# Optimization experiments

Hardware: AMD Instinct MI355X
Metric: run time of the kernel (lower is better)

The kernel has to match this reference:

```python
import jax, jax.numpy as jnp
import numpy as np

D = 1024          # embeddings_dims
HS = 128          # head_size = D // no_of_q_heads(=8)
NKV = 2           # hardcoded self.no_of_kv_heads = 2 (number of query Linear layers)


def apply_rope(x):
    # x: [..., T, d]; pairs of adjacent elements rotated (faithful to RotaryEmbeddings)
    d = x.shape[-1]
    T = x.shape[-2]
    positions = jnp.arange(0, d, 2, dtype=jnp.float32)           # step-2 positions (as in source)
    theta = 10000.0 ** (-2.0 * positions / d)                    # [d/2]
    angles = jnp.arange(T, dtype=jnp.float32)[:, None] * theta[None, :]  # [T, d/2]
    cos, sin = jnp.cos(angles), jnp.sin(angles)
    xr = x.reshape(x.shape[:-1] + (d // 2, 2))
    out = jnp.stack([xr[..., 0] * cos - xr[..., 1] * sin,
                     xr[..., 1] * cos + xr[..., 0] * sin], axis=-1)
    return out.reshape(x.shape)


def setup_inputs() -> dict:
    key = jax.random.key(0)
    k1, k2, k3, k4, k5 = jax.random.split(key, 5)
    B, T = 4, 2048
    x = jax.random.normal(k1, (B, T, D), dtype=jnp.float32)
    s = 1.0 / np.sqrt(D)
    Wq = jax.random.normal(k2, (NKV, HS, D), dtype=jnp.float32) * s  # 2 query Linear layers [out,in]
    Wk = jax.random.normal(k3, (HS, D), dtype=jnp.float32) * s
    Wv = jax.random.normal(k4, (HS, D), dtype=jnp.float32) * s
    Wo = jax.random.normal(k5, (D, NKV * HS), dtype=jnp.float32) * (1.0 / np.sqrt(NKV * HS))
    return {"x": x, "Wq": Wq, "Wk": Wk, "Wv": Wv, "Wo": Wo}


def reference(x, Wq, Wk, Wv, Wo):
    B, T, _ = x.shape
    k = apply_rope(x @ Wk.T)                              # [B,T,HS]
    v = x @ Wv.T                                          # [B,T,HS]
    q = jnp.einsum('btd,hkd->bhtk', x, Wq)                # [B,2,T,HS]
    q = apply_rope(q)
    scale = HS ** (-0.5)
    scores = jnp.einsum('bhtk,bsk->bhts', q, k) * scale   # [B,2,T,T]
    causal = jnp.tril(jnp.ones((T, T), dtype=bool))
    scores = jnp.where(causal, scores, -jnp.inf)
    w = jax.nn.softmax(scores, axis=-1)                   # dropout is identity at eval
    out = jnp.einsum('bhts,bsk->bhtk', w, v)              # [B,2,T,HS]
    out = out.transpose(0, 2, 1, 3).reshape(B, T, NKV * HS)  # concat heads on last dim
    return out @ Wo.T                                     # [B,T,D]
```

## Files before the change

kernel.cpp:

```cpp
#include <hip/hip_runtime.h>
#include <math.h>

#define DD 1024
#define HSZ 128
#define NB 4
#define TT 2048

typedef __attribute__((ext_vector_type(8))) short bf16x8;
typedef __attribute__((ext_vector_type(4))) float f32x4;

typedef __attribute__((address_space(3))) unsigned int lds_u32_t;
typedef __attribute__((address_space(1))) unsigned int glb_u32_t;

__device__ inline void gll16(const void* g, void* l) {
    __builtin_amdgcn_global_load_lds((const glb_u32_t*)g, (lds_u32_t*)l, 16, 0, 0);
}

__device__ inline unsigned short f2bf(float f){
    unsigned u = __builtin_bit_cast(unsigned, f);
    u += 0x7fff + ((u >> 16) & 1);
    return (unsigned short)(u >> 16);
}

__global__ __launch_bounds__(256) void prep_kernel(
    const float* __restrict__ Wq, const float* __restrict__ Wk,
    const float* __restrict__ Wv, const float* __restrict__ Wo,
    unsigned short* __restrict__ Wbp, unsigned short* __restrict__ Wop,
    float2* __restrict__ tab)
{
    int bid = blockIdx.x, tid = threadIdx.x;
    if (bid < 512) {
        int i = bid * 256 + tid;
        int t = i >> 6, j = i & 63;
        float theta = __powf(10000.f, -(float)j * (1.f / 32.f));
        float ang = (float)t * theta;
        tab[i] = make_float2(__cosf(ang), __sinf(ang));
        return;
    }
    const float* s;
    unsigned short* dst;
    if (bid < 768) {
        int gc = (bid - 512) * 256 + tid;
        int tileid = gc >> 10;
        int ct = tileid >> 4, kk = tileid & 15;
        int ch = gc & 1023;
        int ns = ch >> 7, kc = (ch >> 6) & 1, l6 = ch & 63;
        int wrow = ct * 128 + ns * 16 + (l6 & 15);
        int kcol = kk * 64 + kc * 32 + (l6 >> 4) * 8;
        s = (wrow < 256) ? Wq + (size_t)wrow * DD
          : (wrow < 384) ? Wk + (size_t)(wrow - 256) * DD
                         : Wv + (size_t)(wrow - 384) * DD;
        s += kcol;
        dst = Wbp + (size_t)gc * 8;
    } else {
        int gc = (bid - 768) * 256 + tid;
        int tileid = gc >> 10;
        int ct = tileid >> 2, kk = tileid & 3;
        int ch = gc & 1023;
        int ns = ch >> 7, kc = (ch >> 6) & 1, l6 = ch & 63;
        int orow = ct * 128 + ns * 16 + (l6 & 15);
        int kcol = kk * 64 + kc * 32 + (l6 >> 4) * 8;
        s = Wo + (size_t)orow * 256 + kcol;
        dst = Wop + (size_t)gc * 8;
    }
    float4 a = ((const float4*)s)[0];
    float4 c = ((const float4*)s)[1];
    unsigned short o[8] = {f2bf(a.x),f2bf(a.y),f2bf(a.z),f2bf(a.w),
                           f2bf(c.x),f2bf(c.y),f2bf(c.z),f2bf(c.w)};
    *(uint4*)dst = *(const uint4*)o;
}

__global__ __launch_bounds__(256) void qkv_gemm_kernel(
    const float* __restrict__ x,
    const unsigned short* __restrict__ Wbp,
    const float2* __restrict__ tab,
    unsigned short* __restrict__ qo,
    unsigned short* __restrict__ Kp,
    unsigned short* __restrict__ Vp)
{
    int bid = blockIdx.x;
    int rt = bid & 127, ct = bid >> 7;
    int row0 = rt * 64;
    int b = row0 >> 11, t0 = row0 & (TT - 1);
    int tid = threadIdx.x;
    int wave = tid >> 6, lane = tid & 63;
    int mrow = lane & 15, quad = lane >> 4;

    __shared__ unsigned short Bs[2][8192];

    f32x4 acc[8];
    #pragma unroll
    for (int ns = 0; ns < 8; ++ns)
        #pragma unroll
        for (int r = 0; r < 4; ++r) acc[ns][r] = 0.f;

    const float* xrow = x + (size_t)(row0 + wave * 16 + mrow) * DD;

    {
        const unsigned short* wt = Wbp + (size_t)(ct * 16) * 8192;
        #pragma unroll
        for (int u = 0; u < 4; ++u)
            gll16(wt + (size_t)(u * 256 + tid) * 8, &Bs[0][(u * 256 + (tid & 192)) * 8]);
    }

    for (int kk = 0; kk < 16; ++kk) {
        __syncthreads();
        if (kk < 15) {
            const unsigned short* wt = Wbp + (size_t)(ct * 16 + kk + 1) * 8192;
            #pragma unroll
            for (int u = 0; u < 4; ++u)
                gll16(wt + (size_t)(u * 256 + tid) * 8, &Bs[(kk + 1) & 1][(u * 256 + (tid & 192)) * 8]);
        }
        bf16x8 af[2];
        #pragma unroll
        for (int kc = 0; kc < 2; ++kc) {
            const float* s = xrow + kk * 64 + kc * 32 + quad * 8;
            float4 f0 = ((const float4*)s)[0];
            float4 f1 = ((const float4*)s)[1];
            bf16x8 pk;
            pk[0]=(short)f2bf(f0.x); pk[1]=(short)f2bf(f0.y); pk[2]=(short)f2bf(f0.z); pk[3]=(short)f2bf(f0.w);
            pk[4]=(short)f2bf(f1.x); pk[5]=(short)f2bf(f1.y); pk[6]=(short)f2bf(f1.z); pk[7]=(short)f2bf(f1.w);
            af[kc] = pk;
        }
        const unsigned short* Bcur = Bs[kk & 1];
        #pragma unroll
        for (int kc = 0; kc < 2; ++kc)
            #pragma unroll
            for (int ns = 0; ns < 8; ++ns) {
                bf16x8 bb = *(const bf16x8*)(Bcur + ((ns * 2 + kc) * 64 + lane) * 8);
                acc[ns] = __builtin_amdgcn_mfma_f32_16x16x32_bf16(af[kc], bb, acc[ns], 0, 0, 0);
            }
    }

    __syncthreads();

    if (ct < 2) {
        unsigned short* dst = qo + (size_t)(b * 2 + ct) * TT * HSZ;
        #pragma unroll
        for (int ns = 0; ns < 8; ++ns) {
            int colloc = ns * 16 + mrow;
            int pj = colloc >> 1;
            #pragma unroll
            for (int r = 0; r < 4; ++r) {
                int t = t0 + wave * 16 + quad * 4 + r;
                float v = acc[ns][r];
                float vp = __shfl_xor(v, 1, 64);
                float2 cs = tab[t * 64 + pj];
                float outv = ((mrow & 1) == 0) ? (v * cs.x - vp * cs.y)
                                               : (v * cs.x + vp * cs.y);
                dst[(size_t)t * HSZ + colloc] = f2bf(outv);
            }
        }
    } else if (ct == 2) {
        unsigned short* A_ = (unsigned short*)Bs;
        #pragma unroll
        for (int ns = 0; ns < 8; ++ns) {
            int colloc = ns * 16 + mrow;
            int pj = colloc >> 1;
            int chunk = (ns >> 1) * 4 + wave;
            int lph = (ns & 1) * 2 + (mrow >> 3);
            #pragma unroll
            for (int r = 0; r < 4; ++r) {
                int t = t0 + wave * 16 + quad * 4 + r;
                float v = acc[ns][r];
                float vp = __shfl_xor(v, 1, 64);
                float2 cs = tab[t * 64 + pj];
                float outv = ((mrow & 1) == 0) ? (v * cs.x - vp * cs.y)
                                               : (v * cs.x + vp * cs.y);
                A_[chunk * 512 + (lph * 16 + quad * 4 + r) * 8 + (mrow & 7)] = f2bf(outv);
            }
        }
        __syncthreads();
        unsigned short* kd = Kp + (size_t)(b * 32 + (t0 >> 6)) * 8192;
        #pragma unroll
        for (int u = 0; u < 4; ++u)
            *(uint4*)(kd + (u * 256 + tid) * 8) = *(const uint4*)(A_ + (u * 256 + tid) * 8);
    } else {
        unsigned short* A_ = (unsigned short*)Bs;
        #pragma unroll
        for (int ns = 0; ns < 8; ++ns) {
            int chunk = ns * 2 + (wave >> 1);
            int lanep = ((wave & 1) * 2 + (quad >> 1)) * 16 + mrow;
            #pragma unroll
            for (int r = 0; r < 4; ++r)
                A_[chunk * 512 + lanep * 8 + (quad & 1) * 4 + r] = f2bf(acc[ns][r]);
        }
        __syncthreads();
        unsigned short* vd = Vp + (size_t)(b * 32 + (t0 >> 6)) * 8192;
        #pragma unroll
        for (int u = 0; u < 4; ++u)
            *(uint4*)(vd + (u * 256 + tid) * 8) = *(const uint4*)(A_ + (u * 256 + tid) * 8);
    }
}

__global__ __launch_bounds__(256, 2) void attn_mfma_kernel(
    const unsigned short* __restrict__ q,
    const unsigned short* __restrict__ Kp,
    const unsigned short* __restrict__ Vp,
    unsigned short* __restrict__ att)
{
    int bid = blockIdx.x;
    int qt = 63 - (bid >> 3);
    int bh = bid & 7;
    int b = bh >> 1, h = bh & 1;
    int q0 = qt * 32;
    int tid = threadIdx.x;
    int wave = tid >> 6, lane = tid & 63;
    int mrow = lane & 15, quad = lane >> 4;

    __shared__ char raw[66304];
    unsigned short* Psb = (unsigned short*)raw;
    float* Os  = (float*)(raw + 16384);
    float* Ms_ = (float*)(raw + 65536);
    float* Ls_ = Ms_ + 96;

    const unsigned short* qbase = q + (((size_t)(b * 2 + h)) * TT + q0 + mrow) * HSZ + quad * 8;
    bf16x8 qf[2][4];
    #pragma unroll
    for (int u = 0; u < 2; ++u)
        #pragma unroll
        for (int c = 0; c < 4; ++c)
            qf[u][c] = *(const bf16x8*)(qbase + u * 16 * HSZ + 32 * c);

    float mrun[2][4], lrun[2][4];
    f32x4 O[2][8];
    #pragma unroll
    for (int u = 0; u < 2; ++u) {
        #pragma unroll
        for (int r = 0; r < 4; ++r) { mrun[u][r] = -1e30f; lrun[u][r] = 0.f; }
        #pragma unroll
        for (int g = 0; g < 8; ++g)
            #pragma unroll
            for (int r = 0; r < 4; ++r) O[u][g][r] = 0.f;
    }

    const int NT = (qt >> 1) + 1;
    const float scl = 0.08838834764831845f;
    unsigned short* Pw = Psb + wave * 2048;

    for (int j = wave; j < NT; j += 4) {
        const unsigned short* Kt = Kp + (size_t)(b * 32 + j) * 8192;
        const unsigned short* Vt = Vp + (size_t)(b * 32 + j) * 8192;
        int s0 = j * 64;

        f32x4 S[2][4];
        #pragma unroll
        for (int u = 0; u < 2; ++u)
            #pragma unroll
            for (int f = 0; f < 4; ++f)
                #pragma unroll
                for (int r = 0; r < 4; ++r) S[u][f][r] = 0.f;

        #pragma unroll
        for (int c = 0; c < 4; ++c)
            #pragma unroll
            for (int f = 0; f < 4; ++f) {
                bf16x8 bk = *(const bf16x8*)(Kt + ((c * 4 + f) * 64 + lane) * 8);
                S[0][f] = __builtin_amdgcn_mfma_f32_16x16x32_bf16(qf[0][c], bk, S[0][f], 0, 0, 0);
                S[1][f] = __builtin_amdgcn_mfma_f32_16x16x32_bf16(qf[1][c], bk, S[1][f], 0, 0, 0);
            }

        if (j == NT - 1) {
            #pragma unroll
            for (int u = 0; u < 2; ++u)
                #pragma unroll
                for (int f = 0; f < 4; ++f) {
                    int sg = s0 + 16 * f + mrow;
                    #pragma unroll
                    for (int r = 0; r < 4; ++r) {
                        int qg = q0 + u * 16 + quad * 4 + r;
                        S[u][f][r] = (sg <= qg) ? S[u][f][r] * scl : -1e30f;
                    }
                }
        } else {
            #pragma unroll
            for (int u = 0; u < 2; ++u)
                #pragma unroll
                for (int f = 0; f < 4; ++f)
                    #pragma unroll
                    for (int r = 0; r < 4; ++r) S[u][f][r] *= scl;
        }

        #pragma unroll
        for (int u = 0; u < 2; ++u) {
            float al[4];
            #pragma unroll
            for (int r = 0; r < 4; ++r) {
                float v = fmaxf(fmaxf(S[u][0][r], S[u][1][r]), fmaxf(S[u][2][r], S[u][3][r]));
                v = fmaxf(v, __shfl_xor(v, 1, 64));
                v = fmaxf(v, __shfl_xor(v, 2, 64));
                v = fmaxf(v, __shfl_xor(v, 4, 64));
                v = fmaxf(v, __shfl_xor(v, 8, 64));
                float mn = fmaxf(mrun[u][r], v);
                al[r] = __expf(mrun[u][r] - mn);
                mrun[u][r] = mn;
            }
            #pragma unroll
            for (int f = 0; f < 4; ++f)
                #pragma unroll
                for (int r = 0; r < 4; ++r)
                    S[u][f][r] = __expf(S[u][f][r] - mrun[u][r]);
            #pragma unroll
            for (int r = 0; r < 4; ++r) {
                float v = (S[u][0][r] + S[u][1][r]) + (S[u][2][r] + S[u][3][r]);
                v += __shfl_xor(v, 1, 64);
                v += __shfl_xor(v, 2, 64);
                v += __shfl_xor(v, 4, 64);
                v += __shfl_xor(v, 8, 64);
                lrun[u][r] = lrun[u][r] * al[r] + v;
            }
            #pragma unroll
            for (int g = 0; g < 8; ++g) {
                O[u][g][0] *= al[0]; O[u][g][1] *= al[1];
                O[u][g][2] *= al[2]; O[u][g][3] *= al[3];
            }
            #pragma unroll
            for (int f = 0; f < 4; ++f) {
                int p = f >> 1;
                int hi2 = (2 * f + (mrow >> 3)) & 3;
                int jlo = mrow & 7;
                #pragma unroll
                for (int r = 0; r < 4; ++r)
                    Pw[u * 1024 + (p * 64 + hi2 * 16 + quad * 4 + r) * 8 + jlo] = f2bf(S[u][f][r]);
            }
        }

        bf16x8 pa[2][2];
        #pragma unroll
        for (int u = 0; u < 2; ++u)
            #pragma unroll
            for (int p = 0; p < 2; ++p)
                pa[u][p] = *(const bf16x8*)(Pw + u * 1024 + (p * 64 + lane) * 8);

        #pragma unroll
        for (int g = 0; g < 8; ++g)
            #pragma unroll
            for (int p = 0; p < 2; ++p) {
                bf16x8 bv = *(const bf16x8*)(Vt + ((g * 2 + p) * 64 + lane) * 8);
                O[0][g] = __builtin_amdgcn_mfma_f32_16x16x32_bf16(pa[0][p], bv, O[0][g], 0, 0, 0);
                O[1][g] = __builtin_amdgcn_mfma_f32_16x16x32_bf16(pa[1][p], bv, O[1][g], 0, 0, 0);
            }
    }

    if (wave) {
        float* Ow = Os + (wave - 1) * 4096;
        #pragma unroll
        for (int u = 0; u < 2; ++u)
            #pragma unroll
            for (int g = 0; g < 8; ++g)
                #pragma unroll
                for (int r = 0; r < 4; ++r)
                    Ow[(u * 16 + quad * 4 + r) * 128 + g * 16 + mrow] = O[u][g][r];
        if (mrow == 0) {
            #pragma unroll
            for (int u = 0; u < 2; ++u)
                #pragma unroll
                for (int r = 0; r < 4; ++r) {
                    Ms_[(wave - 1) * 32 + u * 16 + quad * 4 + r] = mrun[u][r];
                    Ls_[(wave - 1) * 32 + u * 16 + quad * 4 + r] = lrun[u][r];
                }
        }
    }
    __syncthreads();
    if (wave == 0) {
        unsigned short* ab = att + (((size_t)b * TT + q0) * 2 + h) * 128;
        #pragma unroll
        for (int u = 0; u < 2; ++u) {
            float a0[4], a1[4], a2[4], a3[4], inv[4];
            #pragma unroll
            for (int r = 0; r < 4; ++r) {
                int row = u * 16 + quad * 4 + r;
                float m0 = mrun[u][r], l0 = lrun[u][r];
                float m1 = Ms_[row],      l1 = Ls_[row];
                float m2 = Ms_[32 + row], l2 = Ls_[32 + row];
                float m3 = Ms_[64 + row], l3 = Ls_[64 + row];
                float mM = fmaxf(fmaxf(m0, m1), fmaxf(m2, m3));
                a0[r] = __expf(m0 - mM); a1[r] = __expf(m1 - mM);
                a2[r] = __expf(m2 - mM); a3[r] = __expf(m3 - mM);
                inv[r] = 1.f / (l0 * a0[r] + l1 * a1[r] + l2 * a2[r] + l3 * a3[r]);
            }
            #pragma unroll
            for (int g = 0; g < 8; ++g)
                #pragma unroll
                for (int r = 0; r < 4; ++r) {
                    int row = u * 16 + quad * 4 + r;
                    float o = O[u][g][r] * a0[r]
                            + Os[row * 128 + g * 16 + mrow] * a1[r]
                            + Os[4096 + row * 128 + g * 16 + mrow] * a2[r]
                            + Os[8192 + row * 128 + g * 16 + mrow] * a3[r];
                    ab[(size_t)row * 256 + g * 16 + mrow] = f2bf(o * inv[r]);
                }
        }
    }
}

__global__ __launch_bounds__(256) void outproj_gemm_kernel(
    const unsigned short* __restrict__ attb,
    const unsigned short* __restrict__ Wop,
    float* __restrict__ y)
{
    int bid = blockIdx.x;
    int rt = bid & 127, ct = bid >> 7;
    int row0 = rt * 64;
    int tid = threadIdx.x;
    int wave = tid >> 6, lane = tid & 63;
    int mrow = lane & 15, quad = lane >> 4;

    __shared__ unsigned short Bs[2][8192];

    f32x4 acc[8];
    #pragma unroll
    for (int ns = 0; ns < 8; ++ns)
        #pragma unroll
        for (int r = 0; r < 4; ++r) acc[ns][r] = 0.f;

    const unsigned short* arow = attb + (size_t)(row0 + wave * 16 + mrow) * 256;

    {
        const unsigned short* wt = Wop + (size_t)(ct * 4) * 8192;
        #pragma unroll
        for (int u = 0; u < 4; ++u)
            gll16(wt + (size_t)(u * 256 + tid) * 8, &Bs[0][(u * 256 + (tid & 192)) * 8]);
    }

    for (int kk = 0; kk < 4; ++kk) {
        __syncthreads();
        if (kk < 3) {
            const unsigned short* wt = Wop + (size_t)(ct * 4 + kk + 1) * 8192;
            #pragma unroll
            for (int u = 0; u < 4; ++u)
                gll16(wt + (size_t)(u * 256 + tid) * 8, &Bs[(kk + 1) & 1][(u * 256 + (tid & 192)) * 8]);
        }
        const unsigned short* Bcur = Bs[kk & 1];
        #pragma unroll
        for (int kc = 0; kc < 2; ++kc) {
            bf16x8 af = *(const bf16x8*)(arow + kk * 64 + kc * 32 + quad * 8);
            #pragma unroll
            for (int ns = 0; ns < 8; ++ns) {
                bf16x8 bb = *(const bf16x8*)(Bcur + ((ns * 2 + kc) * 64 + lane) * 8);
                acc[ns] = __builtin_amdgcn_mfma_f32_16x16x32_bf16(af, bb, acc[ns], 0, 0, 0);
            }
        }
    }

    #pragma unroll
    for (int ns = 0; ns < 8; ++ns)
        #pragma unroll
        for (int r = 0; r < 4; ++r) {
            int row = row0 + wave * 16 + quad * 4 + r;
            y[(size_t)row * DD + ct * 128 + ns * 16 + mrow] = acc[ns][r];
        }
}

extern "C" void kernel_launch(void* const* d_in, const int* in_sizes, int n_in,
                              void* d_out, int out_size, void* d_ws, size_t ws_size,
                              hipStream_t stream) {
    const float* x  = (const float*)d_in[0];
    const float* Wq = (const float*)d_in[1];
    const float* Wk = (const float*)d_in[2];
    const float* Wv = (const float*)d_in[3];
    const float* Wo = (const float*)d_in[4];
    float* y = (float*)d_out;

    char* ws = (char*)d_ws;
    unsigned short* at  = (unsigned short*)(ws);
    unsigned short* qo  = (unsigned short*)(ws + 4u  * 1024 * 1024);
    unsigned short* Kp  = (unsigned short*)(ws + 8u  * 1024 * 1024);
    unsigned short* Vp  = (unsigned short*)(ws + 10u * 1024 * 1024);
    unsigned short* Wbp = (unsigned short*)(ws + 12u * 1024 * 1024);
    unsigned short* Wop = (unsigned short*)(ws + 13u * 1024 * 1024);
    float2*         tb  = (float2*)        (ws + 13824u * 1024);

    prep_kernel<<<896, 256, 0, stream>>>(Wq, Wk, Wv, Wo, Wbp, Wop, tb);
    qkv_gemm_kernel<<<512, 256, 0, stream>>>(x, Wbp, tb, qo, Kp, Vp);
    attn_mfma_kernel<<<512, 256, 0, stream>>>(qo, Kp, Vp, at);
    outproj_gemm_kernel<<<1024, 256, 0, stream>>>(at, Wop, y);
}
```

Before: 159.4 us.

## Split attention KV tiles across eight waves with tree merge and swizzled P

The attention kernel now launches 512 threads so eight waves stride over key tiles, and partial softmax states are combined through a three-level LDS tree reduction instead of a four-way merge in one wave. The softmax scale is folded into Q during the QKV epilogue, removing per-tile multiplies. The P staging buffer gets an XOR swizzle to reduce LDS bank conflicts, and the query-tile order is changed to interleave long and short tiles. More waves per block add parallelism for short causal rows but increase register pressure and synchronisation, and the Obuf region overlaps the P buffers, so the merge relies on barriers.

Measured after the change: 200.8 us. +26.0%, slower.

```diff
diff --git a/kernel.cpp b/kernel.cpp
--- a/kernel.cpp
+++ b/kernel.cpp
@@ -21,6 +21,8 @@
     u += 0x7fff + ((u >> 16) & 1);
     return (unsigned short)(u >> 16);
 }
+
+#define QSCL 0.08838834764831845f
 
 __global__ __launch_bounds__(256) void prep_kernel(
     const float* __restrict__ Wq, const float* __restrict__ Wk,
@@ -148,7 +150,7 @@
                 float2 cs = tab[t * 64 + pj];
                 float outv = ((mrow & 1) == 0) ? (v * cs.x - vp * cs.y)
                                                : (v * cs.x + vp * cs.y);
-                dst[(size_t)t * HSZ + colloc] = f2bf(outv);
+                dst[(size_t)t * HSZ + colloc] = f2bf(outv * QSCL);
             }
         }
     } else if (ct == 2) {
@@ -193,14 +195,62 @@
     }
 }
 
-__global__ __launch_bounds__(256, 2) void attn_mfma_kernel(
+#define PUBLISH(BUFI, SLOT)                                                      \
+    {                                                                            \
+        float* buf_ = Obuf + (BUFI) * 4096;                                      \
+        _Pragma("unroll")                                                        \
+        for (int u = 0; u < 2; ++u)                                              \
+            _Pragma("unroll")                                                    \
+            for (int g = 0; g < 8; ++g)                                          \
+                _Pragma("unroll")                                                \
+                for (int r = 0; r < 4; ++r)                                      \
+                    buf_[(u * 16 + quad * 4 + r) * 128 + g * 16 + mrow] = O[u][g][r]; \
+        if (mrow == 0) {                                                         \
+            _Pragma("unroll")                                                    \
+            for (int u = 0; u < 2; ++u)                                          \
+                _Pragma("unroll")                                                \
+                for (int r = 0; r < 4; ++r) {                                    \
+                    Ms_[(SLOT) * 32 + u * 16 + quad * 4 + r] = mrun[u][r];       \
+                    Ls_[(SLOT) * 32 + u * 16 + quad * 4 + r] = lrun[u][r];       \
+                }                                                                \
+        }                                                                        \
+    }
+
+#define MERGE(BUFI, SLOT)                                                        \
+    {                                                                            \
+        float* buf_ = Obuf + (BUFI) * 4096;                                      \
+        float a0[2][4], a1[2][4];                                                \
+        _Pragma("unroll")                                                        \
+        for (int u = 0; u < 2; ++u)                                              \
+            _Pragma("unroll")                                                    \
+            for (int r = 0; r < 4; ++r) {                                        \
+                int row = u * 16 + quad * 4 + r;                                 \
+                float m1 = Ms_[(SLOT) * 32 + row], l1 = Ls_[(SLOT) * 32 + row];  \
+                float mM = fmaxf(mrun[u][r], m1);                                \
+                a0[u][r] = __expf(mrun[u][r] - mM);                              \
+                a1[u][r] = __expf(m1 - mM);                                      \
+                mrun[u][r] = mM;                                                 \
+                lrun[u][r] = lrun[u][r] * a0[u][r] + l1 * a1[u][r];              \
+            }                                                                    \
+        _Pragma("unroll")                                                        \
+        for (int u = 0; u < 2; ++u)                                              \
+            _Pragma("unroll")                                                    \
+            for (int g = 0; g < 8; ++g)                                          \
+                _Pragma("unroll")                                                \
+                for (int r = 0; r < 4; ++r)                                      \
+                    O[u][g][r] = O[u][g][r] * a0[u][r]                           \
+                        + buf_[(u * 16 + quad * 4 + r) * 128 + g * 16 + mrow] * a1[u][r]; \
+    }
+
+__global__ __launch_bounds__(512, 4) void attn_mfma_kernel(
     const unsigned short* __restrict__ q,
     const unsigned short* __restrict__ Kp,
     const unsigned short* __restrict__ Vp,
     unsigned short* __restrict__ att)
 {
     int bid = blockIdx.x;
-    int qt = 63 - (bid >> 3);
+    int t = bid >> 3;
+    int qt = (t < 32) ? 63 - t : t - 32;
     int bh = bid & 7;
     int b = bh >> 1, h = bh & 1;
     int q0 = qt * 32;
@@ -208,11 +258,11 @@
     int wave = tid >> 6, lane = tid & 63;
     int mrow = lane & 15, quad = lane >> 4;
 
-    __shared__ char raw[66304];
+    __shared__ char raw[66560];
     unsigned short* Psb = (unsigned short*)raw;
-    float* Os  = (float*)(raw + 16384);
-    float* Ms_ = (float*)(raw + 65536);
-    float* Ls_ = Ms_ + 96;
+    float* Obuf = (float*)raw;
+    float* Ms_  = (float*)(raw + 65536);
+    float* Ls_  = Ms_ + 128;
 
     const unsigned short* qbase = q + (((size_t)(b * 2 + h)) * TT + q0 + mrow) * HSZ + quad * 8;
     bf16x8 qf[2][4];
@@ -235,10 +285,9 @@
     }
 
     const int NT = (qt >> 1) + 1;
-    const float scl = 0.08838834764831845f;
     unsigned short* Pw = Psb + wave * 2048;
 
-    for (int j = wave; j < NT; j += 4) {
+    for (int j = wave; j < NT; j += 8) {
         const unsigned short* Kt = Kp + (size_t)(b * 32 + j) * 8192;
         const unsigned short* Vt = Vp + (size_t)(b * 32 + j) * 8192;
         int s0 = j * 64;
@@ -269,16 +318,9 @@
                     #pragma unroll
                     for (int r = 0; r < 4; ++r) {
                         int qg = q0 + u * 16 + quad * 4 + r;
-                        S[u][f][r] = (sg <= qg) ? S[u][f][r] * scl : -1e30f;
+                        S[u][f][r] = (sg <= qg) ? S[u][f][r] : -1e30f;
                     }
                 }
-        } else {
-            #pragma unroll
-            for (int u = 0; u < 2; ++u)
-                #pragma unroll
-                for (int f = 0; f < 4; ++f)
-                    #pragma unroll
-                    for (int r = 0; r < 4; ++r) S[u][f][r] *= scl;
         }
 
         #pragma unroll
@@ -319,9 +361,12 @@
                 int p = f >> 1;
                 int hi2 = (2 * f + (mrow >> 3)) & 3;
                 int jlo = mrow & 7;
+                int gx = (quad >> 1) | (hi2 << 1);
                 #pragma unroll
-                for (int r = 0; r < 4; ++r)
-                    Pw[u * 1024 + (p * 64 + hi2 * 16 + quad * 4 + r) * 8 + jlo] = f2bf(S[u][f][r]);
+                for (int r = 0; r < 4; ++r) {
+                    int idx = p * 64 + hi2 * 16 + quad * 4 + r;
+                    Pw[u * 1024 + (idx ^ gx) * 8 + jlo] = f2bf(S[u][f][r]);
+                }
             }
         }
 
@@ -329,8 +374,11 @@
         #pragma unroll
         for (int u = 0; u < 2; ++u)
             #pragma unroll
-            for (int p = 0; p < 2; ++p)
-                pa[u][p] = *(const bf16x8*)(Pw + u * 1024 + (p * 64 + lane) * 8);
+            for (int p = 0; p < 2; ++p) {
+                int li = p * 64 + lane;
+                int si = li ^ ((li >> 3) & 7);
+                pa[u][p] = *(const bf16x8*)(Pw + u * 1024 + si * 8);
+            }
 
         #pragma unroll
         for (int g = 0; g < 8; ++g)
@@ -342,53 +390,29 @@
             }
     }
 
-    if (wave) {
-        float* Ow = Os + (wave - 1) * 4096;
-        #pragma unroll
-        for (int u = 0; u < 2; ++u)
-            #pragma unroll
-            for (int g = 0; g < 8; ++g)
-                #pragma unroll
-                for (int r = 0; r < 4; ++r)
-                    Ow[(u * 16 + quad * 4 + r) * 128 + g * 16 + mrow] = O[u][g][r];
-        if (mrow == 0) {
-            #pragma unroll
-            for (int u = 0; u < 2; ++u)
-                #pragma unroll
-                for (int r = 0; r < 4; ++r) {
-                    Ms_[(wave - 1) * 32 + u * 16 + quad * 4 + r] = mrun[u][r];
-                    Ls_[(wave - 1) * 32 + u * 16 + quad * 4 + r] = lrun[u][r];
-                }
-        }
-    }
+    __syncthreads();
+    if (wave >= 4) PUBLISH(wave - 4, wave - 4);
+    __syncthreads();
+    if (wave < 4)  MERGE(wave, wave);
+    if (wave == 2 || wave == 3) PUBLISH(wave, wave);
+    __syncthreads();
+    if (wave < 2)  MERGE(wave + 2, wave + 2);
+    if (wave == 1) PUBLISH(1, 1);
     __syncthreads();
     if (wave == 0) {
+        MERGE(1, 1);
         unsigned short* ab = att + (((size_t)b * TT + q0) * 2 + h) * 128;
         #pragma unroll
         for (int u = 0; u < 2; ++u) {
-            float a0[4], a1[4], a2[4], a3[4], inv[4];
-            #pragma unroll
-            for (int r = 0; r < 4; ++r) {
-                int row = u * 16 + quad * 4 + r;
-                float m0 = mrun[u][r], l0 = lrun[u][r];
-                float m1 = Ms_[row],      l1 = Ls_[row];
-                float m2 = Ms_[32 + row], l2 = Ls_[32 + row];
-                float m3 = Ms_[64 + row], l3 = Ls_[64 + row];
-                float mM = fmaxf(fmaxf(m0, m1), fmaxf(m2, m3));
-                a0[r] = __expf(m0 - mM); a1[r] = __expf(m1 - mM);
-                a2[r] = __expf(m2 - mM); a3[r] = __expf(m3 - mM);
-                inv[r] = 1.f / (l0 * a0[r] + l1 * a1[r] + l2 * a2[r] + l3 * a3[r]);
-            }
+            float inv[4];
+            #pragma unroll
+            for (int r = 0; r < 4; ++r) inv[r] = 1.f / lrun[u][r];
             #pragma unroll
             for (int g = 0; g < 8; ++g)
                 #pragma unroll
                 for (int r = 0; r < 4; ++r) {
                     int row = u * 16 + quad * 4 + r;
-                    float o = O[u][g][r] * a0[r]
-                            + Os[row * 128 + g * 16 + mrow] * a1[r]
-                            + Os[4096 + row * 128 + g * 16 + mrow] * a2[r]
-                            + Os[8192 + row * 128 + g * 16 + mrow] * a3[r];
-                    ab[(size_t)row * 256 + g * 16 + mrow] = f2bf(o * inv[r]);
+                    ab[(size_t)row * 256 + g * 16 + mrow] = f2bf(O[u][g][r] * inv[r]);
                 }
         }
     }
@@ -473,6 +497,6 @@
 
     prep_kernel<<<896, 256, 0, stream>>>(Wq, Wk, Wv, Wo, Wbp, Wop, tb);
     qkv_gemm_kernel<<<512, 256, 0, stream>>>(x, Wbp, tb, qo, Kp, Vp);
-    attn_mfma_kernel<<<512, 256, 0, stream>>>(qo, Kp, Vp, at);
+    attn_mfma_kernel<<<512, 512, 0, stream>>>(qo, Kp, Vp, at);
     outproj_gemm_kernel<<<1024, 256, 0, stream>>>(at, Wop, y);
 }
```

## Process two KV tiles per wave iteration with single softmax update and swizzled P

Applied to the files above, without the earlier changes.

Each wave now handles a pair of adjacent 64-key tiles per loop iteration, computing both score blocks before one shared online-softmax max/sum/rescale step. This halves the rescale and reduction overhead per key and gives more MFMA work between dependencies. The Q softmax scale is folded into the Q projection epilogue, the P staging buffer in LDS is XOR-swizzled to reduce bank conflicts, and Os now aliases the P buffer, with a barrier added, to shrink LDS. The block order is also changed to interleave light and heavy causal tiles. The launch-bounds occupancy hint is dropped to allow more registers, at the risk of lower occupancy.

Measured after the change: 171.2 us. 7.4% more time.

```diff
diff --git a/kernel.cpp b/kernel.cpp
--- a/kernel.cpp
+++ b/kernel.cpp
@@ -21,6 +21,8 @@
     u += 0x7fff + ((u >> 16) & 1);
     return (unsigned short)(u >> 16);
 }
+
+#define QSCL 0.08838834764831845f
 
 __global__ __launch_bounds__(256) void prep_kernel(
     const float* __restrict__ Wq, const float* __restrict__ Wk,
@@ -148,7 +150,7 @@
                 float2 cs = tab[t * 64 + pj];
                 float outv = ((mrow & 1) == 0) ? (v * cs.x - vp * cs.y)
                                                : (v * cs.x + vp * cs.y);
-                dst[(size_t)t * HSZ + colloc] = f2bf(outv);
+                dst[(size_t)t * HSZ + colloc] = f2bf(outv * QSCL);
             }
         }
     } else if (ct == 2) {
@@ -193,14 +195,15 @@
     }
 }
 
-__global__ __launch_bounds__(256, 2) void attn_mfma_kernel(
+__global__ __launch_bounds__(256) void attn_mfma_kernel(
     const unsigned short* __restrict__ q,
     const unsigned short* __restrict__ Kp,
     const unsigned short* __restrict__ Vp,
     unsigned short* __restrict__ att)
 {
     int bid = blockIdx.x;
-    int qt = 63 - (bid >> 3);
+    int t = bid >> 3;
+    int qt = (t < 32) ? t : 95 - t;
     int bh = bid & 7;
     int b = bh >> 1, h = bh & 1;
     int q0 = qt * 32;
@@ -208,10 +211,10 @@
     int wave = tid >> 6, lane = tid & 63;
     int mrow = lane & 15, quad = lane >> 4;
 
-    __shared__ char raw[66304];
+    __shared__ char raw[49920];
     unsigned short* Psb = (unsigned short*)raw;
-    float* Os  = (float*)(raw + 16384);
-    float* Ms_ = (float*)(raw + 65536);
+    float* Os  = (float*)raw;
+    float* Ms_ = (float*)(raw + 49152);
     float* Ls_ = Ms_ + 96;
 
     const unsigned short* qbase = q + (((size_t)(b * 2 + h)) * TT + q0 + mrow) * HSZ + quad * 8;
@@ -235,32 +238,42 @@
     }
 
     const int NT = (qt >> 1) + 1;
-    const float scl = 0.08838834764831845f;
-    unsigned short* Pw = Psb + wave * 2048;
-
-    for (int j = wave; j < NT; j += 4) {
-        const unsigned short* Kt = Kp + (size_t)(b * 32 + j) * 8192;
-        const unsigned short* Vt = Vp + (size_t)(b * 32 + j) * 8192;
-        int s0 = j * 64;
-
-        f32x4 S[2][4];
+    unsigned short* Pw = Psb + wave * 4096;
+
+    for (int jj = wave * 2; jj < NT; jj += 8) {
+        bool hasB = (jj + 1) < NT;
+        const unsigned short* KtA = Kp + (size_t)(b * 32 + jj) * 8192;
+        const unsigned short* VtA = Vp + (size_t)(b * 32 + jj) * 8192;
+
+        f32x4 SA[2][4], SB[2][4];
         #pragma unroll
         for (int u = 0; u < 2; ++u)
             #pragma unroll
             for (int f = 0; f < 4; ++f)
                 #pragma unroll
-                for (int r = 0; r < 4; ++r) S[u][f][r] = 0.f;
+                for (int r = 0; r < 4; ++r) { SA[u][f][r] = 0.f; SB[u][f][r] = 0.f; }
 
         #pragma unroll
         for (int c = 0; c < 4; ++c)
             #pragma unroll
             for (int f = 0; f < 4; ++f) {
-                bf16x8 bk = *(const bf16x8*)(Kt + ((c * 4 + f) * 64 + lane) * 8);
-                S[0][f] = __builtin_amdgcn_mfma_f32_16x16x32_bf16(qf[0][c], bk, S[0][f], 0, 0, 0);
-                S[1][f] = __builtin_amdgcn_mfma_f32_16x16x32_bf16(qf[1][c], bk, S[1][f], 0, 0, 0);
-            }
-
-        if (j == NT - 1) {
+                bf16x8 bk = *(const bf16x8*)(KtA + ((c * 4 + f) * 64 + lane) * 8);
+                SA[0][f] = __builtin_amdgcn_mfma_f32_16x16x32_bf16(qf[0][c], bk, SA[0][f], 0, 0, 0);
+                SA[1][f] = __builtin_amdgcn_mfma_f32_16x16x32_bf16(qf[1][c], bk, SA[1][f], 0, 0, 0);
+            }
+        if (hasB) {
+            #pragma unroll
+            for (int c = 0; c < 4; ++c)
+                #pragma unroll
+                for (int f = 0; f < 4; ++f) {
+                    bf16x8 bk = *(const bf16x8*)(KtA + 8192 + ((c * 4 + f) * 64 + lane) * 8);
+                    SB[0][f] = __builtin_amdgcn_mfma_f32_16x16x32_bf16(qf[0][c], bk, SB[0][f], 0, 0, 0);
+                    SB[1][f] = __builtin_amdgcn_mfma_f32_16x16x32_bf16(qf[1][c], bk, SB[1][f], 0, 0, 0);
+                }
+        }
+
+        if (!hasB) {
+            int s0 = jj * 64;
             #pragma unroll
             for (int u = 0; u < 2; ++u)
                 #pragma unroll
@@ -269,79 +282,142 @@
                     #pragma unroll
                     for (int r = 0; r < 4; ++r) {
                         int qg = q0 + u * 16 + quad * 4 + r;
-                        S[u][f][r] = (sg <= qg) ? S[u][f][r] * scl : -1e30f;
+                        SA[u][f][r] = (sg <= qg) ? SA[u][f][r] : -1e30f;
                     }
                 }
-        } else {
+        } else if (jj + 2 == NT) {
+            int s0 = (jj + 1) * 64;
             #pragma unroll
             for (int u = 0; u < 2; ++u)
                 #pragma unroll
-                for (int f = 0; f < 4; ++f)
+                for (int f = 0; f < 4; ++f) {
+                    int sg = s0 + 16 * f + mrow;
                     #pragma unroll
-                    for (int r = 0; r < 4; ++r) S[u][f][r] *= scl;
-        }
-
-        #pragma unroll
-        for (int u = 0; u < 2; ++u) {
-            float al[4];
+                    for (int r = 0; r < 4; ++r) {
+                        int qg = q0 + u * 16 + quad * 4 + r;
+                        SB[u][f][r] = (sg <= qg) ? SB[u][f][r] : -1e30f;
+                    }
+                }
+        }
+
+        float al[2][4];
+        #pragma unroll
+        for (int u = 0; u < 2; ++u)
             #pragma unroll
             for (int r = 0; r < 4; ++r) {
-                float v = fmaxf(fmaxf(S[u][0][r], S[u][1][r]), fmaxf(S[u][2][r], S[u][3][r]));
+                float v = fmaxf(fmaxf(SA[u][0][r], SA[u][1][r]), fmaxf(SA[u][2][r], SA[u][3][r]));
+                if (hasB) {
+                    float w = fmaxf(fmaxf(SB[u][0][r], SB[u][1][r]), fmaxf(SB[u][2][r], SB[u][3][r]));
+                    v = fmaxf(v, w);
+                }
                 v = fmaxf(v, __shfl_xor(v, 1, 64));
                 v = fmaxf(v, __shfl_xor(v, 2, 64));
                 v = fmaxf(v, __shfl_xor(v, 4, 64));
                 v = fmaxf(v, __shfl_xor(v, 8, 64));
                 float mn = fmaxf(mrun[u][r], v);
-                al[r] = __expf(mrun[u][r] - mn);
+                al[u][r] = __expf(mrun[u][r] - mn);
                 mrun[u][r] = mn;
             }
+        #pragma unroll
+        for (int u = 0; u < 2; ++u)
             #pragma unroll
             for (int f = 0; f < 4; ++f)
                 #pragma unroll
                 for (int r = 0; r < 4; ++r)
-                    S[u][f][r] = __expf(S[u][f][r] - mrun[u][r]);
+                    SA[u][f][r] = __expf(SA[u][f][r] - mrun[u][r]);
+        if (hasB) {
+            #pragma unroll
+            for (int u = 0; u < 2; ++u)
+                #pragma unroll
+                for (int f = 0; f < 4; ++f)
+                    #pragma unroll
+                    for (int r = 0; r < 4; ++r)
+                        SB[u][f][r] = __expf(SB[u][f][r] - mrun[u][r]);
+        }
+        #pragma unroll
+        for (int u = 0; u < 2; ++u)
             #pragma unroll
             for (int r = 0; r < 4; ++r) {
-                float v = (S[u][0][r] + S[u][1][r]) + (S[u][2][r] + S[u][3][r]);
+                float v = (SA[u][0][r] + SA[u][1][r]) + (SA[u][2][r] + SA[u][3][r]);
+                if (hasB)
+                    v += (SB[u][0][r] + SB[u][1][r]) + (SB[u][2][r] + SB[u][3][r]);
                 v += __shfl_xor(v, 1, 64);
                 v += __shfl_xor(v, 2, 64);
                 v += __shfl_xor(v, 4, 64);
                 v += __shfl_xor(v, 8, 64);
-                lrun[u][r] = lrun[u][r] * al[r] + v;
-            }
+                lrun[u][r] = lrun[u][r] * al[u][r] + v;
+            }
+        #pragma unroll
+        for (int u = 0; u < 2; ++u)
             #pragma unroll
             for (int g = 0; g < 8; ++g) {
-                O[u][g][0] *= al[0]; O[u][g][1] *= al[1];
-                O[u][g][2] *= al[2]; O[u][g][3] *= al[3];
-            }
+                O[u][g][0] *= al[u][0]; O[u][g][1] *= al[u][1];
+                O[u][g][2] *= al[u][2]; O[u][g][3] *= al[u][3];
+            }
+
+        #pragma unroll
+        for (int u = 0; u < 2; ++u)
             #pragma unroll
             for (int f = 0; f < 4; ++f) {
                 int p = f >> 1;
                 int hi2 = (2 * f + (mrow >> 3)) & 3;
                 int jlo = mrow & 7;
-                #pragma unroll
-                for (int r = 0; r < 4; ++r)
-                    Pw[u * 1024 + (p * 64 + hi2 * 16 + quad * 4 + r) * 8 + jlo] = f2bf(S[u][f][r]);
-            }
-        }
-
-        bf16x8 pa[2][2];
-        #pragma unroll
-        for (int u = 0; u < 2; ++u)
-            #pragma unroll
-            for (int p = 0; p < 2; ++p)
-                pa[u][p] = *(const bf16x8*)(Pw + u * 1024 + (p * 64 + lane) * 8);
+                int gx = (quad >> 1) | (hi2 << 1);
+                #pragma unroll
+                for (int r = 0; r < 4; ++r) {
+                    int idx = p * 64 + hi2 * 16 + quad * 4 + r;
+                    Pw[u * 1024 + (idx ^ gx) * 8 + jlo] = f2bf(SA[u][f][r]);
+                }
+            }
+        if (hasB) {
+            #pragma unroll
+            for (int u = 0; u < 2; ++u)
+                #pragma unroll
+                for (int f = 0; f < 4; ++f) {
+                    int p = f >> 1;
+                    int hi2 = (2 * f + (mrow >> 3)) & 3;
+                    int jlo = mrow & 7;
+                    int gx = (quad >> 1) | (hi2 << 1);
+                    #pragma unroll
+                    for (int r = 0; r < 4; ++r) {
+                        int idx = p * 64 + hi2 * 16 + quad * 4 + r;
+                        Pw[2048 + u * 1024 + (idx ^ gx) * 8 + jlo] = f2bf(SB[u][f][r]);
+                    }
+                }
+        }
+
+        bf16x8 paA[2][2], paB[2][2];
+        #pragma unroll
+        for (int u = 0; u < 2; ++u)
+            #pragma unroll
+            for (int p = 0; p < 2; ++p) {
+                int li = p * 64 + lane;
+                int si = li ^ ((li >> 3) & 7);
+                paA[u][p] = *(const bf16x8*)(Pw + u * 1024 + si * 8);
+                if (hasB) paB[u][p] = *(const bf16x8*)(Pw + 2048 + u * 1024 + si * 8);
+            }
 
         #pragma unroll
         for (int g = 0; g < 8; ++g)
             #pragma unroll
             for (int p = 0; p < 2; ++p) {
-                bf16x8 bv = *(const bf16x8*)(Vt + ((g * 2 + p) * 64 + lane) * 8);
-                O[0][g] = __builtin_amdgcn_mfma_f32_16x16x32_bf16(pa[0][p], bv, O[0][g], 0, 0, 0);
-                O[1][g] = __builtin_amdgcn_mfma_f32_16x16x32_bf16(pa[1][p], bv, O[1][g], 0, 0, 0);
-            }
-    }
-
+                bf16x8 bv = *(const bf16x8*)(VtA + ((g * 2 + p) * 64 + lane) * 8);
+                O[0][g] = __builtin_amdgcn_mfma_f32_16x16x32_bf16(paA[0][p], bv, O[0][g], 0, 0, 0);
+                O[1][g] = __builtin_amdgcn_mfma_f32_16x16x32_bf16(paA[1][p], bv, O[1][g], 0, 0, 0);
+            }
+        if (hasB) {
+            #pragma unroll
+            for (int g = 0; g < 8; ++g)
+                #pragma unroll
+                for (int p = 0; p < 2; ++p) {
+                    bf16x8 bv = *(const bf16x8*)(VtA + 8192 + ((g * 2 + p) * 64 + lane) * 8);
+                    O[0][g] = __builtin_amdgcn_mfma_f32_16x16x32_bf16(paB[0][p], bv, O[0][g], 0, 0, 0);
+                    O[1][g] = __builtin_amdgcn_mfma_f32_16x16x32_bf16(paB[1][p], bv, O[1][g], 0, 0, 0);
+                }
+        }
+    }
+
+    __syncthreads();
     if (wave) {
         float* Ow = Os + (wave - 1) * 4096;
         #pragma unroll
```

## Merge QKV column tiles into 512-thread blocks and fold softmax scale into Q

Applied to the files above, without the earlier changes.

The QKV GEMM now runs 256 blocks of 512 threads. Each block computes two 128-column tiles that share the same 64 x rows, so the fp32 x load and bf16 conversion are amortised across more output columns (though each wave still loads x itself). The attention scale is multiplied into Q at the GEMM epilogue, which removes the per-tile scale multiply in the attention loop. The cost is larger LDS use per block and fewer blocks in flight. Rounding Q to bf16 after scaling changes precision slightly.

New measurement: 168.8 us. 1.06x slower.

```diff
diff --git a/kernel.cpp b/kernel.cpp
--- a/kernel.cpp
+++ b/kernel.cpp
@@ -21,6 +21,8 @@
     u += 0x7fff + ((u >> 16) & 1);
     return (unsigned short)(u >> 16);
 }
+
+#define QSCL 0.08838834764831845f
 
 __global__ __launch_bounds__(256) void prep_kernel(
     const float* __restrict__ Wq, const float* __restrict__ Wk,
@@ -70,7 +72,7 @@
     *(uint4*)dst = *(const uint4*)o;
 }
 
-__global__ __launch_bounds__(256) void qkv_gemm_kernel(
+__global__ __launch_bounds__(512) void qkv_gemm_kernel(
     const float* __restrict__ x,
     const unsigned short* __restrict__ Wbp,
     const float2* __restrict__ tab,
@@ -79,14 +81,16 @@
     unsigned short* __restrict__ Vp)
 {
     int bid = blockIdx.x;
-    int rt = bid & 127, ct = bid >> 7;
+    int rt = bid & 127, ctp = bid >> 7;
     int row0 = rt * 64;
     int b = row0 >> 11, t0 = row0 & (TT - 1);
     int tid = threadIdx.x;
     int wave = tid >> 6, lane = tid & 63;
+    int wgrp = wave & 3, chalf = wave >> 2;
+    int ct = ctp * 2 + chalf;
     int mrow = lane & 15, quad = lane >> 4;
 
-    __shared__ unsigned short Bs[2][8192];
+    __shared__ unsigned short Bs[2][16384];
 
     f32x4 acc[8];
     #pragma unroll
@@ -94,22 +98,32 @@
         #pragma unroll
         for (int r = 0; r < 4; ++r) acc[ns][r] = 0.f;
 
-    const float* xrow = x + (size_t)(row0 + wave * 16 + mrow) * DD;
+    const float* xrow = x + (size_t)(row0 + wgrp * 16 + mrow) * DD;
 
     {
-        const unsigned short* wt = Wbp + (size_t)(ct * 16) * 8192;
-        #pragma unroll
-        for (int u = 0; u < 4; ++u)
-            gll16(wt + (size_t)(u * 256 + tid) * 8, &Bs[0][(u * 256 + (tid & 192)) * 8]);
+        #pragma unroll
+        for (int u = 0; u < 4; ++u) {
+            int cb = u * 512 + wave * 64;
+            int ch = cb >> 10;
+            int within = cb & 1023;
+            const unsigned short* wt = Wbp
+                + (size_t)((ctp * 2 + ch) * 16) * 8192 + (size_t)(within + lane) * 8;
+            gll16(wt, &Bs[0][cb * 8]);
+        }
     }
 
     for (int kk = 0; kk < 16; ++kk) {
         __syncthreads();
         if (kk < 15) {
-            const unsigned short* wt = Wbp + (size_t)(ct * 16 + kk + 1) * 8192;
-            #pragma unroll
-            for (int u = 0; u < 4; ++u)
-                gll16(wt + (size_t)(u * 256 + tid) * 8, &Bs[(kk + 1) & 1][(u * 256 + (tid & 192)) * 8]);
+            #pragma unroll
+            for (int u = 0; u < 4; ++u) {
+                int cb = u * 512 + wave * 64;
+                int ch = cb >> 10;
+                int within = cb & 1023;
+                const unsigned short* wt = Wbp
+                    + (size_t)((ctp * 2 + ch) * 16 + kk + 1) * 8192 + (size_t)(within + lane) * 8;
+                gll16(wt, &Bs[(kk + 1) & 1][cb * 8]);
+            }
         }
         bf16x8 af[2];
         #pragma unroll
@@ -122,7 +136,7 @@
             pk[4]=(short)f2bf(f1.x); pk[5]=(short)f2bf(f1.y); pk[6]=(short)f2bf(f1.z); pk[7]=(short)f2bf(f1.w);
             af[kc] = pk;
         }
-        const unsigned short* Bcur = Bs[kk & 1];
+        const unsigned short* Bcur = &Bs[kk & 1][chalf * 8192];
         #pragma unroll
         for (int kc = 0; kc < 2; ++kc)
             #pragma unroll
@@ -134,7 +148,7 @@
 
     __syncthreads();
 
-    if (ct < 2) {
+    if (ctp == 0) {
         unsigned short* dst = qo + (size_t)(b * 2 + ct) * TT * HSZ;
         #pragma unroll
         for (int ns = 0; ns < 8; ++ns) {
@@ -142,26 +156,26 @@
             int pj = colloc >> 1;
             #pragma unroll
             for (int r = 0; r < 4; ++r) {
-                int t = t0 + wave * 16 + quad * 4 + r;
+                int t = t0 + wgrp * 16 + quad * 4 + r;
                 float v = acc[ns][r];
                 float vp = __shfl_xor(v, 1, 64);
                 float2 cs = tab[t * 64 + pj];
                 float outv = ((mrow & 1) == 0) ? (v * cs.x - vp * cs.y)
                                                : (v * cs.x + vp * cs.y);
-                dst[(size_t)t * HSZ + colloc] = f2bf(outv);
-            }
-        }
-    } else if (ct == 2) {
-        unsigned short* A_ = (unsigned short*)Bs;
+                dst[(size_t)t * HSZ + colloc] = f2bf(outv * QSCL);
+            }
+        }
+    } else if (chalf == 0) {
+        unsigned short* A_ = &Bs[0][0];
         #pragma unroll
         for (int ns = 0; ns < 8; ++ns) {
             int colloc = ns * 16 + mrow;
             int pj = colloc >> 1;
-            int chunk = (ns >> 1) * 4 + wave;
+            int chunk = (ns >> 1) * 4 + wgrp;
             int lph = (ns & 1) * 2 + (mrow >> 3);
             #pragma unroll
             for (int r = 0; r < 4; ++r) {
-                int t = t0 + wave * 16 + quad * 4 + r;
+                int t = t0 + wgrp * 16 + quad * 4 + r;
                 float v = acc[ns][r];
                 float vp = __shfl_xor(v, 1, 64);
                 float2 cs = tab[t * 64 + pj];
@@ -170,26 +184,31 @@
                 A_[chunk * 512 + (lph * 16 + quad * 4 + r) * 8 + (mrow & 7)] = f2bf(outv);
             }
         }
-        __syncthreads();
-        unsigned short* kd = Kp + (size_t)(b * 32 + (t0 >> 6)) * 8192;
-        #pragma unroll
-        for (int u = 0; u < 4; ++u)
-            *(uint4*)(kd + (u * 256 + tid) * 8) = *(const uint4*)(A_ + (u * 256 + tid) * 8);
     } else {
-        unsigned short* A_ = (unsigned short*)Bs;
+        unsigned short* A_ = &Bs[1][0];
         #pragma unroll
         for (int ns = 0; ns < 8; ++ns) {
-            int chunk = ns * 2 + (wave >> 1);
-            int lanep = ((wave & 1) * 2 + (quad >> 1)) * 16 + mrow;
+            int chunk = ns * 2 + (wgrp >> 1);
+            int lanep = ((wgrp & 1) * 2 + (quad >> 1)) * 16 + mrow;
             #pragma unroll
             for (int r = 0; r < 4; ++r)
                 A_[chunk * 512 + lanep * 8 + (quad & 1) * 4 + r] = f2bf(acc[ns][r]);
         }
-        __syncthreads();
-        unsigned short* vd = Vp + (size_t)(b * 32 + (t0 >> 6)) * 8192;
-        #pragma unroll
-        for (int u = 0; u < 4; ++u)
-            *(uint4*)(vd + (u * 256 + tid) * 8) = *(const uint4*)(A_ + (u * 256 + tid) * 8);
+    }
+    __syncthreads();
+    if (ctp == 1) {
+        int tid4 = tid & 255;
+        if (chalf == 0) {
+            unsigned short* kd = Kp + (size_t)(b * 32 + (t0 >> 6)) * 8192;
+            #pragma unroll
+            for (int u = 0; u < 4; ++u)
+                *(uint4*)(kd + (u * 256 + tid4) * 8) = *(const uint4*)(&Bs[0][0] + (u * 256 + tid4) * 8);
+        } else {
+            unsigned short* vd = Vp + (size_t)(b * 32 + (t0 >> 6)) * 8192;
+            #pragma unroll
+            for (int u = 0; u < 4; ++u)
+                *(uint4*)(vd + (u * 256 + tid4) * 8) = *(const uint4*)(&Bs[1][0] + (u * 256 + tid4) * 8);
+        }
     }
 }
 
@@ -235,7 +254,6 @@
     }
 
     const int NT = (qt >> 1) + 1;
-    const float scl = 0.08838834764831845f;
     unsigned short* Pw = Psb + wave * 2048;
 
     for (int j = wave; j < NT; j += 4) {
@@ -269,16 +287,9 @@
                     #pragma unroll
                     for (int r = 0; r < 4; ++r) {
                         int qg = q0 + u * 16 + quad * 4 + r;
-                        S[u][f][r] = (sg <= qg) ? S[u][f][r] * scl : -1e30f;
+                        S[u][f][r] = (sg <= qg) ? S[u][f][r] : -1e30f;
                     }
                 }
-        } else {
-            #pragma unroll
-            for (int u = 0; u < 2; ++u)
-                #pragma unroll
-                for (int f = 0; f < 4; ++f)
-                    #pragma unroll
-                    for (int r = 0; r < 4; ++r) S[u][f][r] *= scl;
         }
 
         #pragma unroll
@@ -472,7 +483,7 @@
     float2*         tb  = (float2*)        (ws + 13824u * 1024);
 
     prep_kernel<<<896, 256, 0, stream>>>(Wq, Wk, Wv, Wo, Wbp, Wop, tb);
-    qkv_gemm_kernel<<<512, 256, 0, stream>>>(x, Wbp, tb, qo, Kp, Vp);
+    qkv_gemm_kernel<<<256, 512, 0, stream>>>(x, Wbp, tb, qo, Kp, Vp);
     attn_mfma_kernel<<<512, 256, 0, stream>>>(qo, Kp, Vp, at);
     outproj_gemm_kernel<<<1024, 256, 0, stream>>>(at, Wop, y);
 }
```
